# Performance work log

Measured on AMD Instinct MI355X. Metric: run time of the kernel, lower is better.

The kernel has to match this reference:

```python
import jax, jax.numpy as jnp
import numpy as np

N = 100000
E = 1600000
F = 128
H = 128
EPS = 1e-5
NEG_SLOPE = 0.2


def setup_inputs() -> dict:
    key = jax.random.key(0)
    ks = jax.random.split(key, 24)
    def nrm(k, shape, scale=0.05):
        return jax.random.normal(k, shape, dtype=jnp.float32) * scale
    inp = {
        'x': jax.random.normal(ks[0], (N, F), dtype=jnp.float32),
        'edge_index': jax.random.randint(ks[1], (2, E), 0, N, dtype=jnp.int64),
        # conv 0: F -> H
        'W0': nrm(ks[2], (F, H)), 'asrc0': nrm(ks[3], (H,)), 'adst0': nrm(ks[4], (H,)), 'b0': nrm(ks[5], (H,)),
        # convs 1..4 (middle): H -> H, stacked
        'Wm': nrm(ks[6], (4, H, H)), 'asrcm': nrm(ks[7], (4, H)), 'adstm': nrm(ks[8], (4, H)), 'bm': nrm(ks[9], (4, H)),
        # conv 5 (last): H -> H
        'W5': nrm(ks[10], (H, H)), 'asrc5': nrm(ks[11], (H,)), 'adst5': nrm(ks[12], (H,)), 'b5': nrm(ks[13], (H,)),
        # batchnorm affine params for all 6 layers
        'gammas': jnp.ones((6, H), dtype=jnp.float32), 'betas': jnp.zeros((6, H), dtype=jnp.float32),
        # residual transform F -> H and output layer H -> F
        'Wr': nrm(ks[14], (F, H)), 'br': nrm(ks[15], (H,)),
        'Wo': nrm(ks[16], (H, F)), 'bo': nrm(ks[17], (F,)),
    }
    return inp


def _gat_layer(x, W, a_src, a_dst, b, src, dst):
    # PyG GATConv, heads=1: h = x W; e_ij = LeakyReLU(a_src.h_j + a_dst.h_i)
    # softmax over incoming edges of each destination node, scatter-add aggregate.
    h = x @ W                              # [N, H]
    s = h @ a_src                          # [N]
    d = h @ a_dst                          # [N]
    e = jax.nn.leaky_relu(s[src] + d[dst], NEG_SLOPE)   # [E']
    m = jax.ops.segment_max(e, dst, num_segments=N)      # per-dst max (self-loops guarantee nonempty)
    p = jnp.exp(e - m[dst])
    z = jax.ops.segment_sum(p, dst, num_segments=N)
    alpha = p / z[dst]                     # [E']
    out = jax.ops.segment_sum(alpha[:, None] * h[src], dst, num_segments=N)
    return out + b


def _bn(x, g, beta):
    # BatchNorm1d, training mode (batch statistics, biased variance)
    mu = x.mean(axis=0)
    var = x.var(axis=0)
    return g * (x - mu) * jax.lax.rsqrt(var + EPS) + beta


def reference(x, edge_index, W0, asrc0, adst0, b0, Wm, asrcm, adstm, bm,
              W5, asrc5, adst5, b5, gammas, betas, Wr, br, Wo, bo):
    # add self-loops (PyG GATConv default)
    loops = jnp.arange(N, dtype=edge_index.dtype)
    src = jnp.concatenate([edge_index[0], loops])
    dst = jnp.concatenate([edge_index[1], loops])

    residual = x @ Wr + br
    # first 5 convs: conv -> bn -> relu -> (dropout=identity) -> +residual
    layer_params = [(W0, asrc0, adst0, b0)] + [
        (Wm[i], asrcm[i], adstm[i], bm[i]) for i in range(4)
    ]
    h = x
    for i, (W, a_s, a_d, b) in enumerate(layer_params):
        h = _gat_layer(h, W, a_s, a_d, b, src, dst)
        h = jax.nn.relu(_bn(h, gammas[i], betas[i]))
        h = h + residual
        residual = h
    # last conv -> bn -> out_layer
    h = _gat_layer(h, W5, asrc5, adst5, b5, src, dst)
    h = _bn(h, gammas[5], betas[5])
    return h @ Wo + bo
```

## Files before the change

### kernel.cpp

```cpp
#include <hip/hip_runtime.h>

#define NF 128
#define EPS 1e-5f
#define SLOPE 0.2f

typedef __attribute__((ext_vector_type(8))) short bf16x8;
typedef __attribute__((ext_vector_type(4))) float f32x4;

static __device__ __forceinline__ unsigned short f2bf(float f) {
  unsigned int u = __builtin_bit_cast(unsigned int, f);
  u += 0x7fffu + ((u >> 16) & 1u);
  return (unsigned short)(u >> 16);
}
static __device__ __forceinline__ float bf2f(unsigned short s) {
  return __builtin_bit_cast(float, (unsigned int)s << 16);
}
static __device__ __forceinline__ float bflo(unsigned int u) {
  return __builtin_bit_cast(float, u << 16);
}
static __device__ __forceinline__ float bfhi(unsigned int u) {
  return __builtin_bit_cast(float, u & 0xffff0000u);
}
static __device__ __forceinline__ unsigned int pack2(float a, float b) {
  return (unsigned int)f2bf(a) | ((unsigned int)f2bf(b) << 16);
}


__global__ void k_init_counts(int* counts, int n) {
  int i = blockIdx.x * 256 + threadIdx.x;
  if (i < n) counts[i] = 1;
}

__global__ void k_count(const int* __restrict__ dst, int* __restrict__ counts,
                        int* __restrict__ pos, int e) {
  int i = blockIdx.x * 256 + threadIdx.x;
  if (i < e) pos[i] = atomicAdd(&counts[dst[i]], 1);
}

__global__ void k_scan_part(const int* __restrict__ counts, int* __restrict__ partials, int n) {
  __shared__ int sd[256];
  int base = blockIdx.x * 2048;
  int sum = 0;
  for (int i = threadIdx.x; i < 2048; i += 256) {
    int idx = base + i;
    sum += (idx < n) ? counts[idx] : 0;
  }
  sd[threadIdx.x] = sum;
  __syncthreads();
  for (int s = 128; s > 0; s >>= 1) {
    if (threadIdx.x < s) sd[threadIdx.x] += sd[threadIdx.x + s];
    __syncthreads();
  }
  if (threadIdx.x == 0) partials[blockIdx.x] = sd[0];
}

__global__ void k_scan_mid(int* partials, int nb) {
  if (threadIdx.x == 0 && blockIdx.x == 0) {
    int acc = 0;
    for (int b = 0; b < nb; b++) { int v = partials[b]; partials[b] = acc; acc += v; }
  }
}

__global__ void k_scan_final(const int* __restrict__ counts, const int* __restrict__ partials,
                             int* __restrict__ offsets, int n) {
  __shared__ int sd[256];
  int t = threadIdx.x;
  int base = blockIdx.x * 2048;
  int local[8];
  int sum = 0;
#pragma unroll
  for (int j = 0; j < 8; j++) {
    int idx = base + t * 8 + j;
    int v = (idx < n) ? counts[idx] : 0;
    local[j] = sum;
    sum += v;
  }
  sd[t] = sum;
  __syncthreads();
  for (int st = 1; st < 256; st <<= 1) {
    int v = 0;
    if (t >= st) v = sd[t - st];
    __syncthreads();
    if (t >= st) sd[t] += v;
    __syncthreads();
  }
  int tb = partials[blockIdx.x] + (t > 0 ? sd[t - 1] : 0);
#pragma unroll
  for (int j = 0; j < 8; j++) {
    int idx = base + t * 8 + j;
    if (idx < n) offsets[idx] = tb + local[j];
  }
}

__global__ void k_selfloop(int* __restrict__ offsets, int* __restrict__ csr, int n, int total) {
  int i = blockIdx.x * 256 + threadIdx.x;
  if (i < n) csr[offsets[i]] = i;
  if (i == 0) offsets[n] = total;
}

__global__ void k_fill(const int* __restrict__ src, const int* __restrict__ dst,
                       const int* __restrict__ offsets, const int* __restrict__ pos,
                       int* __restrict__ csr, int e) {
  int i = blockIdx.x * 256 + threadIdx.x;
  if (i < e) csr[offsets[dst[i]] + pos[i]] = src[i];
}


__global__ void k_f32_to_bf16(const float* __restrict__ x, unsigned short* __restrict__ o,
                              int n, int np) {
  int i = blockIdx.x * 256 + threadIdx.x;
  if (i >= np * (NF / 4)) return;
  int row = i >> 5;
  ushort4 ov;
  if (row < n) {
    float4 v = ((const float4*)x)[i];
    ov = make_ushort4(f2bf(v.x), f2bf(v.y), f2bf(v.z), f2bf(v.w));
  } else {
    ov = make_ushort4(0, 0, 0, 0);
  }
  ((ushort4*)o)[i] = ov;
}

__global__ void k_wt(const float* __restrict__ W0, const float* __restrict__ Wm,
                     const float* __restrict__ W5, const float* __restrict__ Wr,
                     const float* __restrict__ Wo, unsigned short* __restrict__ Wt) {
  int idx = blockIdx.x * 256 + threadIdx.x;
  if (idx >= 8 * NF * NF) return;
  int mat = idx >> 14;
  int rem = idx & 16383;
  int r = rem >> 7;
  int k = rem & 127;
  const float* W = (mat == 0) ? W0
                 : (mat <= 4) ? Wm + (size_t)(mat - 1) * NF * NF
                 : (mat == 5) ? W5
                 : (mat == 6) ? Wr : Wo;
  Wt[idx] = f2bf(W[k * NF + r]);
}


template <int MODE>
__global__ __launch_bounds__(256) void k_gemm_mfma(
    const unsigned short* __restrict__ A, const unsigned short* __restrict__ Wt,
    const float* __restrict__ asrc, const float* __restrict__ adst,
    const float* __restrict__ bias, unsigned short* __restrict__ Cb,
    float* __restrict__ Cf, float* __restrict__ sv, float* __restrict__ dv, int n) {
  int w = threadIdx.x >> 6;
  int l = threadIdx.x & 63;
  int lr = l & 15, lh = l >> 4;
  int row0 = blockIdx.x * 128 + w * 32;

  const unsigned short* Ab = A + (size_t)(row0 + lr) * NF + lh * 8;
  bf16x8 af[2][4];
#pragma unroll
  for (int m = 0; m < 2; m++)
#pragma unroll
    for (int kk = 0; kk < 4; kk++)
      af[m][kk] = *(const bf16x8*)(Ab + m * 16 * NF + kk * 32);

  f32x4 acc[2][8];
#pragma unroll
  for (int m = 0; m < 2; m++)
#pragma unroll
    for (int nn = 0; nn < 8; nn++) acc[m][nn] = (f32x4){0.f, 0.f, 0.f, 0.f};

  const unsigned short* Bb = Wt + (size_t)lr * NF + lh * 8;
#pragma unroll
  for (int kk = 0; kk < 4; kk++) {
    bf16x8 bfr[8];
#pragma unroll
    for (int nn = 0; nn < 8; nn++)
      bfr[nn] = *(const bf16x8*)(Bb + nn * 16 * NF + kk * 32);
#pragma unroll
    for (int m = 0; m < 2; m++)
#pragma unroll
      for (int nn = 0; nn < 8; nn++)
        acc[m][nn] = __builtin_amdgcn_mfma_f32_16x16x32_bf16(af[m][kk], bfr[nn], acc[m][nn], 0, 0, 0);
  }

  if (MODE == 0) {
    float as[8], ad[8];
#pragma unroll
    for (int nn = 0; nn < 8; nn++) {
      as[nn] = asrc[nn * 16 + lr];
      ad[nn] = adst[nn * 16 + lr];
    }
#pragma unroll
    for (int m = 0; m < 2; m++) {
#pragma unroll
      for (int r = 0; r < 4; r++) {
        int row = row0 + m * 16 + lh * 4 + r;
        float sp = 0.f, dp = 0.f;
#pragma unroll
        for (int nn = 0; nn < 8; nn++) {
          float v = acc[m][nn][r];
          sp += v * as[nn];
          dp += v * ad[nn];
          Cb[(size_t)row * NF + nn * 16 + lr] = f2bf(v);
        }
#pragma unroll
        for (int mk = 8; mk > 0; mk >>= 1) {
          sp += __shfl_xor(sp, mk);
          dp += __shfl_xor(dp, mk);
        }
        if (lr == 0) { sv[row] = sp; dv[row] = dp; }
      }
    }
  } else if (MODE == 1) {
    float bcol[8];
#pragma unroll
    for (int nn = 0; nn < 8; nn++) bcol[nn] = bias[nn * 16 + lr];
#pragma unroll
    for (int m = 0; m < 2; m++)
#pragma unroll
      for (int r = 0; r < 4; r++) {
        int row = row0 + m * 16 + lh * 4 + r;
        if (row < n) {
#pragma unroll
          for (int nn = 0; nn < 8; nn++)
            Cf[(size_t)row * NF + nn * 16 + lr] = acc[m][nn][r] + bcol[nn];
        }
      }
  } else {
    float bcol[8];
#pragma unroll
    for (int nn = 0; nn < 8; nn++) bcol[nn] = bias[nn * 16 + lr];
#pragma unroll
    for (int m = 0; m < 2; m++)
#pragma unroll
      for (int r = 0; r < 4; r++) {
        int row = row0 + m * 16 + lh * 4 + r;
#pragma unroll
        for (int nn = 0; nn < 8; nn++)
          Cb[(size_t)row * NF + nn * 16 + lr] = f2bf(acc[m][nn][r] + bcol[nn]);
      }
  }
}


__global__ __launch_bounds__(256) void k_attn_gather(
    const float* __restrict__ sv, const float* __restrict__ dv,
    const int* __restrict__ offs, const int* __restrict__ csr,
    const unsigned short* __restrict__ hbf, const float* __restrict__ bias,
    unsigned short* __restrict__ aggb, float* __restrict__ pstat, int n) {
  int w = threadIdx.x >> 6, l = threadIdx.x & 63;
  int ll = l & 15, g = l >> 4;
  int node0 = blockIdx.x * 16 + w * 4;
  float ps[8] = {0.f, 0.f, 0.f, 0.f, 0.f, 0.f, 0.f, 0.f};
  float qs[8] = {0.f, 0.f, 0.f, 0.f, 0.f, 0.f, 0.f, 0.f};
  float4 bv0 = *(const float4*)&bias[8 * ll];
  float4 bv1 = *(const float4*)&bias[8 * ll + 4];

  for (int ni = 0; ni < 4; ni++) {
    int node = node0 + ni;
    if (node >= n) break;
    int o0 = offs[node], o1 = offs[node + 1];
    int deg = o1 - o0;
    float di = dv[node];
    float a[8] = {0.f, 0.f, 0.f, 0.f, 0.f, 0.f, 0.f, 0.f};

    if (deg <= 64) {
      bool valid = l < deg;
      int srcj = valid ? csr[o0 + l] : 0;
      float ev = valid ? sv[srcj] + di : -1e30f;
      ev = ev >= 0.f ? ev : SLOPE * ev;
      float m = ev;
#pragma unroll
      for (int k2 = 32; k2 > 0; k2 >>= 1) m = fmaxf(m, __shfl_xor(m, k2));
      float pe = valid ? __expf(ev - m) : 0.f;
      float z = pe;
#pragma unroll
      for (int k2 = 32; k2 > 0; k2 >>= 1) z += __shfl_xor(z, k2);
      float wj = pe / z;

      for (int t2 = 0; t2 < deg; t2 += 8) {
        int ta = t2 + g;
        int tb = t2 + 4 + g;
        int sA = __shfl(srcj, ta);
        int sB = __shfl(srcj, tb);
        float wA = __shfl(wj, ta);
        float wB = __shfl(wj, tb);
        uint4 hA = *(const uint4*)(hbf + (size_t)sA * NF + 8 * ll);
        uint4 hB = *(const uint4*)(hbf + (size_t)sB * NF + 8 * ll);
        a[0] += wA * bflo(hA.x) + wB * bflo(hB.x);
        a[1] += wA * bfhi(hA.x) + wB * bfhi(hB.x);
        a[2] += wA * bflo(hA.y) + wB * bflo(hB.y);
        a[3] += wA * bfhi(hA.y) + wB * bfhi(hB.y);
        a[4] += wA * bflo(hA.z) + wB * bflo(hB.z);
        a[5] += wA * bfhi(hA.z) + wB * bfhi(hB.z);
        a[6] += wA * bflo(hA.w) + wB * bflo(hB.w);
        a[7] += wA * bfhi(hA.w) + wB * bfhi(hB.w);
      }
    } else {
      float m = -1e30f;
      for (int j = o0 + l; j < o1; j += 64) {
        float ev = sv[csr[j]] + di;
        ev = ev >= 0.f ? ev : SLOPE * ev;
        m = fmaxf(m, ev);
      }
#pragma unroll
      for (int k2 = 32; k2 > 0; k2 >>= 1) m = fmaxf(m, __shfl_xor(m, k2));
      float z = 0.f;
      for (int j = o0 + l; j < o1; j += 64) {
        float ev = sv[csr[j]] + di;
        ev = ev >= 0.f ? ev : SLOPE * ev;
        z += __expf(ev - m);
      }
#pragma unroll
      for (int k2 = 32; k2 > 0; k2 >>= 1) z += __shfl_xor(z, k2);
      float inv = 1.f / z;
      for (int t2 = 0; t2 < deg; t2 += 4) {
        int tt = t2 + g;
        if (tt < deg) {
          int sI = csr[o0 + tt];
          float ev = sv[sI] + di;
          ev = ev >= 0.f ? ev : SLOPE * ev;
          float wI = __expf(ev - m) * inv;
          uint4 hv = *(const uint4*)(hbf + (size_t)sI * NF + 8 * ll);
          a[0] += wI * bflo(hv.x);
          a[1] += wI * bfhi(hv.x);
          a[2] += wI * bflo(hv.y);
          a[3] += wI * bfhi(hv.y);
          a[4] += wI * bflo(hv.z);
          a[5] += wI * bfhi(hv.z);
          a[6] += wI * bflo(hv.w);
          a[7] += wI * bfhi(hv.w);
        }
      }
    }
#pragma unroll
    for (int j = 0; j < 8; j++) {
      a[j] += __shfl_xor(a[j], 16);
      a[j] += __shfl_xor(a[j], 32);
    }
    if (g == 0) {
      a[0] += bv0.x; a[1] += bv0.y; a[2] += bv0.z; a[3] += bv0.w;
      a[4] += bv1.x; a[5] += bv1.y; a[6] += bv1.z; a[7] += bv1.w;
      uint4 ov;
      ov.x = pack2(a[0], a[1]);
      ov.y = pack2(a[2], a[3]);
      ov.z = pack2(a[4], a[5]);
      ov.w = pack2(a[6], a[7]);
      *(uint4*)(aggb + (size_t)node * NF + 8 * ll) = ov;
#pragma unroll
      for (int j = 0; j < 8; j++) { ps[j] += a[j]; qs[j] += a[j] * a[j]; }
    }
  }

  __shared__ float red[4][16][17];
  if (g == 0) {
#pragma unroll
    for (int j = 0; j < 8; j++) {
      red[w][ll][j] = ps[j];
      red[w][ll][8 + j] = qs[j];
    }
  }
  __syncthreads();
  int t = threadIdx.x;
  int c = t & 127, kind = t >> 7;
  int li = c >> 3, sj = (c & 7) + 8 * kind;
  float v = red[0][li][sj] + red[1][li][sj] + red[2][li][sj] + red[3][li][sj];
  atomicAdd(&pstat[(blockIdx.x & 63) * 256 + t], v);
}


__global__ void k_bnfinal(float* __restrict__ pstat, const float* __restrict__ gamma,
                          const float* __restrict__ beta, float* __restrict__ scsh,
                          float ninv) {
  __shared__ float tot[256];
  int t = threadIdx.x;
  float v = 0.f;
  for (int s2 = 0; s2 < 64; s2++) {
    v += pstat[s2 * 256 + t];
    pstat[s2 * 256 + t] = 0.f;
  }
  tot[t] = v;
  __syncthreads();
  if (t < 128) {
    float mu = tot[t] * ninv;
    float var = tot[128 + t] * ninv - mu * mu;
    float sc = gamma[t] * rsqrtf(var + EPS);
    scsh[t] = sc;
    scsh[128 + t] = beta[t] - mu * sc;
  }
}


template <int RELU_RES>
__global__ __launch_bounds__(256) void k_bn_apply(
    const unsigned short* __restrict__ agg, const float* __restrict__ scsh,
    const unsigned short* __restrict__ res, unsigned short* __restrict__ out, int n) {
  int cq = threadIdx.x & 31;
  int c0 = cq * 4;
  float sc0 = scsh[c0], sc1 = scsh[c0 + 1], sc2 = scsh[c0 + 2], sc3 = scsh[c0 + 3];
  float sh0 = scsh[128 + c0], sh1 = scsh[128 + c0 + 1], sh2 = scsh[128 + c0 + 2],
        sh3 = scsh[128 + c0 + 3];
  for (int r = blockIdx.x * 8 + (threadIdx.x >> 5); r < n; r += gridDim.x * 8) {
    size_t i = (size_t)r * 32 + cq;
    ushort4 av = ((const ushort4*)agg)[i];
    float v0 = bf2f(av.x) * sc0 + sh0;
    float v1 = bf2f(av.y) * sc1 + sh1;
    float v2 = bf2f(av.z) * sc2 + sh2;
    float v3 = bf2f(av.w) * sc3 + sh3;
    if (RELU_RES) {
      ushort4 rv = ((const ushort4*)res)[i];
      v0 = fmaxf(v0, 0.f) + bf2f(rv.x);
      v1 = fmaxf(v1, 0.f) + bf2f(rv.y);
      v2 = fmaxf(v2, 0.f) + bf2f(rv.z);
      v3 = fmaxf(v3, 0.f) + bf2f(rv.w);
    }
    ((ushort4*)out)[i] = make_ushort4(f2bf(v0), f2bf(v1), f2bf(v2), f2bf(v3));
  }
}


extern "C" void kernel_launch(void* const* d_in, const int* in_sizes, int n_in,
                              void* d_out, int out_size, void* d_ws, size_t ws_size,
                              hipStream_t stream) {
  (void)n_in; (void)out_size; (void)ws_size;
  const float* x     = (const float*)d_in[0];
  const int*   ei    = (const int*)d_in[1];
  const float* W0    = (const float*)d_in[2];
  const float* asrc0 = (const float*)d_in[3];
  const float* adst0 = (const float*)d_in[4];
  const float* b0    = (const float*)d_in[5];
  const float* Wm    = (const float*)d_in[6];
  const float* asrcm = (const float*)d_in[7];
  const float* adstm = (const float*)d_in[8];
  const float* bm    = (const float*)d_in[9];
  const float* W5    = (const float*)d_in[10];
  const float* asrc5 = (const float*)d_in[11];
  const float* adst5 = (const float*)d_in[12];
  const float* b5    = (const float*)d_in[13];
  const float* gammas= (const float*)d_in[14];
  const float* betas = (const float*)d_in[15];
  const float* Wr    = (const float*)d_in[16];
  const float* br    = (const float*)d_in[17];
  const float* Wo    = (const float*)d_in[18];
  const float* bo    = (const float*)d_in[19];

  const int n = in_sizes[0] / NF;
  const int np = (n + 127) & ~127;
  const int e = in_sizes[1] / 2;
  const int tot = e + n;
  const int* srcp = ei;
  const int* dstp = ei + e;

  char* w = (char*)d_ws;
  auto carve = [&](size_t bytes) {
    char* p = w;
    w += (bytes + 255) & ~(size_t)255;
    return p;
  };
  unsigned short* h_bf    = (unsigned short*)carve((size_t)np * NF * 2);
  unsigned short* hlin_bf = (unsigned short*)carve((size_t)np * NF * 2);
  unsigned short* res_bf  = (unsigned short*)carve((size_t)np * NF * 2);
  unsigned short* agg_bf  = (unsigned short*)carve((size_t)n * NF * 2);
  unsigned short* Wt      = (unsigned short*)carve((size_t)8 * NF * NF * 2);
  float* sv      = (float*)carve((size_t)np * 4);
  float* dv      = (float*)carve((size_t)np * 4);
  int*   csr     = (int*)carve((size_t)tot * 4);
  int*   offsets = (int*)carve((size_t)(n + 1) * 4);
  int*   counts  = (int*)carve((size_t)n * 4);
  int*   pos     = (int*)carve((size_t)e * 4);
  int*   partials= (int*)carve(64 * 4);
  float* pstat   = (float*)carve(64 * 256 * 4);
  float* scsh    = (float*)carve(256 * 4);

  int nb = (n + 2047) / 2048;

  k_wt<<<(8 * NF * NF + 255) / 256, 256, 0, stream>>>(W0, Wm, W5, Wr, Wo, Wt);
  k_f32_to_bf16<<<(np * (NF / 4) + 255) / 256, 256, 0, stream>>>(x, h_bf, n, np);

  k_init_counts<<<(n + 255) / 256, 256, 0, stream>>>(counts, n);
  k_count<<<(e + 255) / 256, 256, 0, stream>>>(dstp, counts, pos, e);
  k_scan_part<<<nb, 256, 0, stream>>>(counts, partials, n);
  k_scan_mid<<<1, 64, 0, stream>>>(partials, nb);
  k_scan_final<<<nb, 256, 0, stream>>>(counts, partials, offsets, n);
  k_selfloop<<<(n + 255) / 256, 256, 0, stream>>>(offsets, csr, n, tot);
  k_fill<<<(e + 255) / 256, 256, 0, stream>>>(srcp, dstp, offsets, pos, csr, e);

  hipMemsetAsync(pstat, 0, 64 * 256 * 4, stream);

  int gemm_grid = np / 128;

  k_gemm_mfma<2><<<gemm_grid, 256, 0, stream>>>(h_bf, Wt + 6 * NF * NF, nullptr, nullptr,
                                                br, res_bf, nullptr, nullptr, nullptr, n);

  for (int L = 0; L < 6; L++) {
    const float *als, *ald, *bl;
    if (L == 0)      { als = asrc0; ald = adst0; bl = b0; }
    else if (L <= 4) { als = asrcm + (L - 1) * NF; ald = adstm + (L - 1) * NF; bl = bm + (L - 1) * NF; }
    else             { als = asrc5; ald = adst5; bl = b5; }

    k_gemm_mfma<0><<<gemm_grid, 256, 0, stream>>>(h_bf, Wt + (size_t)L * NF * NF,
                                                  als, ald, nullptr, hlin_bf, nullptr, sv, dv, n);
    k_attn_gather<<<(n + 15) / 16, 256, 0, stream>>>(sv, dv, offsets, csr, hlin_bf, bl,
                                                     agg_bf, pstat, n);
    k_bnfinal<<<1, 256, 0, stream>>>(pstat, gammas + L * NF, betas + L * NF, scsh, 1.0f / n);

    if (L < 5) {
      k_bn_apply<1><<<1024, 256, 0, stream>>>(agg_bf, scsh, (L == 0) ? res_bf : h_bf, h_bf, n);
    } else {
      k_bn_apply<0><<<1024, 256, 0, stream>>>(agg_bf, scsh, nullptr, hlin_bf, n);
      k_gemm_mfma<1><<<gemm_grid, 256, 0, stream>>>(hlin_bf, Wt + 7 * NF * NF, nullptr, nullptr,
                                                    bo, nullptr, (float*)d_out, nullptr, nullptr, n);
    }
  }
}
```

Baseline: 883.9 us.

## Fuse BN apply into next GEMM, split CSR fill, unroll gather by four

The batchnorm-apply, ReLU and residual-add step now runs inside the A-operand load of the next layer's MFMA GEMM. That GEMM also writes the updated h back for the residual, so the standalone bn_apply kernel and one full read/write pass per layer go away. The final output GEMM applies BN directly from the aggregate buffer. The CSR fill is split into 8 passes over destination ranges to make scattered writes more local, at the cost of rereading the edge list 8 times. The gather loop is unrolled to four neighbours per iteration for more memory-level parallelism. agg_bf is padded to np rows because the fused GEMM reads the padded tail rows.

```diff
diff --git a/kernel.cpp b/kernel.cpp
--- a/kernel.cpp
+++ b/kernel.cpp
@@ -98,11 +98,14 @@
   if (i == 0) offsets[n] = total;
 }
 
-__global__ void k_fill(const int* __restrict__ src, const int* __restrict__ dst,
-                       const int* __restrict__ offsets, const int* __restrict__ pos,
-                       int* __restrict__ csr, int e) {
+__global__ void k_fill_pass(const int* __restrict__ src, const int* __restrict__ dst,
+                            const int* __restrict__ offsets, const int* __restrict__ pos,
+                            int* __restrict__ csr, int e, int lo, int hi) {
   int i = blockIdx.x * 256 + threadIdx.x;
-  if (i < e) csr[offsets[dst[i]] + pos[i]] = src[i];
+  if (i < e) {
+    int d = dst[i];
+    if (d >= lo && d < hi) csr[offsets[d] + pos[i]] = src[i];
+  }
 }
 
 
@@ -143,19 +146,63 @@
     const unsigned short* __restrict__ A, const unsigned short* __restrict__ Wt,
     const float* __restrict__ asrc, const float* __restrict__ adst,
     const float* __restrict__ bias, unsigned short* __restrict__ Cb,
-    float* __restrict__ Cf, float* __restrict__ sv, float* __restrict__ dv, int n) {
+    float* __restrict__ Cf, float* __restrict__ sv, float* __restrict__ dv, int n,
+    const unsigned short* __restrict__ agg, const unsigned short* __restrict__ res,
+    const float* __restrict__ scsh, unsigned short* __restrict__ hout) {
   int w = threadIdx.x >> 6;
   int l = threadIdx.x & 63;
   int lr = l & 15, lh = l >> 4;
   int row0 = blockIdx.x * 128 + w * 32;
 
-  const unsigned short* Ab = A + (size_t)(row0 + lr) * NF + lh * 8;
   bf16x8 af[2][4];
-#pragma unroll
-  for (int m = 0; m < 2; m++)
-#pragma unroll
-    for (int kk = 0; kk < 4; kk++)
-      af[m][kk] = *(const bf16x8*)(Ab + m * 16 * NF + kk * 32);
+  if (MODE <= 2) {
+    const unsigned short* Ab = A + (size_t)(row0 + lr) * NF + lh * 8;
+#pragma unroll
+    for (int m = 0; m < 2; m++)
+#pragma unroll
+      for (int kk = 0; kk < 4; kk++)
+        af[m][kk] = *(const bf16x8*)(Ab + m * 16 * NF + kk * 32);
+  } else {
+#pragma unroll
+    for (int kk = 0; kk < 4; kk++) {
+      int c0 = lh * 8 + kk * 32;
+      float4 scA = *(const float4*)&scsh[c0];
+      float4 scB = *(const float4*)&scsh[c0 + 4];
+      float4 shA = *(const float4*)&scsh[128 + c0];
+      float4 shB = *(const float4*)&scsh[128 + c0 + 4];
+#pragma unroll
+      for (int m = 0; m < 2; m++) {
+        size_t base = (size_t)(row0 + lr + m * 16) * NF + c0;
+        uint4 ag = *(const uint4*)(agg + base);
+        float v0 = bflo(ag.x) * scA.x + shA.x;
+        float v1 = bfhi(ag.x) * scA.y + shA.y;
+        float v2 = bflo(ag.y) * scA.z + shA.z;
+        float v3 = bfhi(ag.y) * scA.w + shA.w;
+        float v4 = bflo(ag.z) * scB.x + shB.x;
+        float v5 = bfhi(ag.z) * scB.y + shB.y;
+        float v6 = bflo(ag.w) * scB.z + shB.z;
+        float v7 = bfhi(ag.w) * scB.w + shB.w;
+        if (MODE == 3) {
+          uint4 rs = *(const uint4*)(res + base);
+          v0 = fmaxf(v0, 0.f) + bflo(rs.x);
+          v1 = fmaxf(v1, 0.f) + bfhi(rs.x);
+          v2 = fmaxf(v2, 0.f) + bflo(rs.y);
+          v3 = fmaxf(v3, 0.f) + bfhi(rs.y);
+          v4 = fmaxf(v4, 0.f) + bflo(rs.z);
+          v5 = fmaxf(v5, 0.f) + bfhi(rs.z);
+          v6 = fmaxf(v6, 0.f) + bflo(rs.w);
+          v7 = fmaxf(v7, 0.f) + bfhi(rs.w);
+        }
+        uint4 hv;
+        hv.x = pack2(v0, v1);
+        hv.y = pack2(v2, v3);
+        hv.z = pack2(v4, v5);
+        hv.w = pack2(v6, v7);
+        if (MODE == 3) *(uint4*)(hout + base) = hv;
+        af[m][kk] = __builtin_bit_cast(bf16x8, hv);
+      }
+    }
+  }
 
   f32x4 acc[2][8];
 #pragma unroll
@@ -177,7 +224,7 @@
         acc[m][nn] = __builtin_amdgcn_mfma_f32_16x16x32_bf16(af[m][kk], bfr[nn], acc[m][nn], 0, 0, 0);
   }
 
-  if (MODE == 0) {
+  if (MODE == 0 || MODE == 3) {
     float as[8], ad[8];
 #pragma unroll
     for (int nn = 0; nn < 8; nn++) {
@@ -205,7 +252,7 @@
         if (lr == 0) { sv[row] = sp; dv[row] = dp; }
       }
     }
-  } else if (MODE == 1) {
+  } else if (MODE == 1 || MODE == 4) {
     float bcol[8];
 #pragma unroll
     for (int nn = 0; nn < 8; nn++) bcol[nn] = bias[nn * 16 + lr];
@@ -272,23 +319,28 @@
       for (int k2 = 32; k2 > 0; k2 >>= 1) z += __shfl_xor(z, k2);
       float wj = pe / z;
 
-      for (int t2 = 0; t2 < deg; t2 += 8) {
-        int ta = t2 + g;
-        int tb = t2 + 4 + g;
+      for (int t2 = 0; t2 < deg; t2 += 16) {
+        int ta = t2 + g, tb = t2 + 4 + g, tc = t2 + 8 + g, td = t2 + 12 + g;
         int sA = __shfl(srcj, ta);
         int sB = __shfl(srcj, tb);
+        int sC = __shfl(srcj, tc);
+        int sD = __shfl(srcj, td);
         float wA = __shfl(wj, ta);
         float wB = __shfl(wj, tb);
+        float wC = __shfl(wj, tc);
+        float wD = __shfl(wj, td);
         uint4 hA = *(const uint4*)(hbf + (size_t)sA * NF + 8 * ll);
         uint4 hB = *(const uint4*)(hbf + (size_t)sB * NF + 8 * ll);
-        a[0] += wA * bflo(hA.x) + wB * bflo(hB.x);
-        a[1] += wA * bfhi(hA.x) + wB * bfhi(hB.x);
-        a[2] += wA * bflo(hA.y) + wB * bflo(hB.y);
-        a[3] += wA * bfhi(hA.y) + wB * bfhi(hB.y);
-        a[4] += wA * bflo(hA.z) + wB * bflo(hB.z);
-        a[5] += wA * bfhi(hA.z) + wB * bfhi(hB.z);
-        a[6] += wA * bflo(hA.w) + wB * bflo(hB.w);
-        a[7] += wA * bfhi(hA.w) + wB * bfhi(hB.w);
+        uint4 hC = *(const uint4*)(hbf + (size_t)sC * NF + 8 * ll);
+        uint4 hD = *(const uint4*)(hbf + (size_t)sD * NF + 8 * ll);
+        a[0] += wA * bflo(hA.x) + wB * bflo(hB.x) + wC * bflo(hC.x) + wD * bflo(hD.x);
+        a[1] += wA * bfhi(hA.x) + wB * bfhi(hB.x) + wC * bfhi(hC.x) + wD * bfhi(hD.x);
+        a[2] += wA * bflo(hA.y) + wB * bflo(hB.y) + wC * bflo(hC.y) + wD * bflo(hD.y);
+        a[3] += wA * bfhi(hA.y) + wB * bfhi(hB.y) + wC * bfhi(hC.y) + wD * bfhi(hD.y);
+        a[4] += wA * bflo(hA.z) + wB * bflo(hB.z) + wC * bflo(hC.z) + wD * bflo(hD.z);
+        a[5] += wA * bfhi(hA.z) + wB * bfhi(hB.z) + wC * bfhi(hC.z) + wD * bfhi(hD.z);
+        a[6] += wA * bflo(hA.w) + wB * bflo(hB.w) + wC * bflo(hC.w) + wD * bflo(hD.w);
+        a[7] += wA * bfhi(hA.w) + wB * bfhi(hB.w) + wC * bfhi(hC.w) + wD * bfhi(hD.w);
       }
     } else {
       float m = -1e30f;
@@ -381,34 +433,6 @@
     float sc = gamma[t] * rsqrtf(var + EPS);
     scsh[t] = sc;
     scsh[128 + t] = beta[t] - mu * sc;
-  }
-}
-
-
-template <int RELU_RES>
-__global__ __launch_bounds__(256) void k_bn_apply(
-    const unsigned short* __restrict__ agg, const float* __restrict__ scsh,
-    const unsigned short* __restrict__ res, unsigned short* __restrict__ out, int n) {
-  int cq = threadIdx.x & 31;
-  int c0 = cq * 4;
-  float sc0 = scsh[c0], sc1 = scsh[c0 + 1], sc2 = scsh[c0 + 2], sc3 = scsh[c0 + 3];
-  float sh0 = scsh[128 + c0], sh1 = scsh[128 + c0 + 1], sh2 = scsh[128 + c0 + 2],
-        sh3 = scsh[128 + c0 + 3];
-  for (int r = blockIdx.x * 8 + (threadIdx.x >> 5); r < n; r += gridDim.x * 8) {
-    size_t i = (size_t)r * 32 + cq;
-    ushort4 av = ((const ushort4*)agg)[i];
-    float v0 = bf2f(av.x) * sc0 + sh0;
-    float v1 = bf2f(av.y) * sc1 + sh1;
-    float v2 = bf2f(av.z) * sc2 + sh2;
-    float v3 = bf2f(av.w) * sc3 + sh3;
-    if (RELU_RES) {
-      ushort4 rv = ((const ushort4*)res)[i];
-      v0 = fmaxf(v0, 0.f) + bf2f(rv.x);
-      v1 = fmaxf(v1, 0.f) + bf2f(rv.y);
-      v2 = fmaxf(v2, 0.f) + bf2f(rv.z);
-      v3 = fmaxf(v3, 0.f) + bf2f(rv.w);
-    }
-    ((ushort4*)out)[i] = make_ushort4(f2bf(v0), f2bf(v1), f2bf(v2), f2bf(v3));
   }
 }
 
@@ -454,7 +478,7 @@
   unsigned short* h_bf    = (unsigned short*)carve((size_t)np * NF * 2);
   unsigned short* hlin_bf = (unsigned short*)carve((size_t)np * NF * 2);
   unsigned short* res_bf  = (unsigned short*)carve((size_t)np * NF * 2);
-  unsigned short* agg_bf  = (unsigned short*)carve((size_t)n * NF * 2);
+  unsigned short* agg_bf  = (unsigned short*)carve((size_t)np * NF * 2);
   unsigned short* Wt      = (unsigned short*)carve((size_t)8 * NF * NF * 2);
   float* sv      = (float*)carve((size_t)np * 4);
   float* dv      = (float*)carve((size_t)np * 4);
@@ -477,14 +501,23 @@
   k_scan_mid<<<1, 64, 0, stream>>>(partials, nb);
   k_scan_final<<<nb, 256, 0, stream>>>(counts, partials, offsets, n);
   k_selfloop<<<(n + 255) / 256, 256, 0, stream>>>(offsets, csr, n, tot);
-  k_fill<<<(e + 255) / 256, 256, 0, stream>>>(srcp, dstp, offsets, pos, csr, e);
+  {
+    const int NPASS = 8;
+    int step = (n + NPASS - 1) / NPASS;
+    for (int p = 0; p < NPASS; p++) {
+      int lo = p * step;
+      int hi = min(n, lo + step);
+      k_fill_pass<<<(e + 255) / 256, 256, 0, stream>>>(srcp, dstp, offsets, pos, csr, e, lo, hi);
+    }
+  }
 
   hipMemsetAsync(pstat, 0, 64 * 256 * 4, stream);
 
   int gemm_grid = np / 128;
 
   k_gemm_mfma<2><<<gemm_grid, 256, 0, stream>>>(h_bf, Wt + 6 * NF * NF, nullptr, nullptr,
-                                                br, res_bf, nullptr, nullptr, nullptr, n);
+                                                br, res_bf, nullptr, nullptr, nullptr, n,
+                                                nullptr, nullptr, nullptr, nullptr);
 
   for (int L = 0; L < 6; L++) {
     const float *als, *ald, *bl;
@@ -492,18 +525,23 @@
     else if (L <= 4) { als = asrcm + (L - 1) * NF; ald = adstm + (L - 1) * NF; bl = bm + (L - 1) * NF; }
     else             { als = asrc5; ald = adst5; bl = b5; }
 
-    k_gemm_mfma<0><<<gemm_grid, 256, 0, stream>>>(h_bf, Wt + (size_t)L * NF * NF,
-                                                  als, ald, nullptr, hlin_bf, nullptr, sv, dv, n);
+    if (L == 0) {
+      k_gemm_mfma<0><<<gemm_grid, 256, 0, stream>>>(h_bf, Wt, als, ald, nullptr, hlin_bf,
+                                                    nullptr, sv, dv, n,
+                                                    nullptr, nullptr, nullptr, nullptr);
+    } else {
+      const unsigned short* resb = (L == 1) ? res_bf : h_bf;
+      k_gemm_mfma<3><<<gemm_grid, 256, 0, stream>>>(nullptr, Wt + (size_t)L * NF * NF,
+                                                    als, ald, nullptr, hlin_bf, nullptr, sv, dv, n,
+                                                    agg_bf, resb, scsh, h_bf);
+    }
+
     k_attn_gather<<<(n + 15) / 16, 256, 0, stream>>>(sv, dv, offsets, csr, hlin_bf, bl,
                                                      agg_bf, pstat, n);
     k_bnfinal<<<1, 256, 0, stream>>>(pstat, gammas + L * NF, betas + L * NF, scsh, 1.0f / n);
-
-    if (L < 5) {
-      k_bn_apply<1><<<1024, 256, 0, stream>>>(agg_bf, scsh, (L == 0) ? res_bf : h_bf, h_bf, n);
-    } else {
-      k_bn_apply<0><<<1024, 256, 0, stream>>>(agg_bf, scsh, nullptr, hlin_bf, n);
-      k_gemm_mfma<1><<<gemm_grid, 256, 0, stream>>>(hlin_bf, Wt + 7 * NF * NF, nullptr, nullptr,
-                                                    bo, nullptr, (float*)d_out, nullptr, nullptr, n);
-    }
-  }
-}
+  }
+
+  k_gemm_mfma<4><<<gemm_grid, 256, 0, stream>>>(nullptr, Wt + 7 * NF * NF, nullptr, nullptr,
+                                                bo, nullptr, (float*)d_out, nullptr, nullptr, n,
+                                                agg_bf, nullptr, scsh, nullptr);
+}
```

Result: no change. 892.9 us (+1.0%).
